# Optimization experiments

Hardware: AMD Instinct MI355X
Metric: run time of the kernel (lower is better)

## Reference

```python
import jax, jax.numpy as jnp
import numpy as np

EPS = 1e-7  # keras.backend.epsilon()


def setup_inputs() -> dict:
    key = jax.random.key(0)
    kx, kw, ku = jax.random.split(key, 3)
    B, S, F = 16, 4096, 512
    x = jax.random.normal(kx, (B, S, F), dtype=jnp.float32)
    # glorot-uniform-scaled weights
    limW = np.sqrt(6.0 / (F + F)).astype(np.float32)
    W = jax.random.uniform(kw, (F, F), dtype=jnp.float32, minval=-limW, maxval=limW)
    b = jnp.zeros((F,), dtype=jnp.float32)
    limu = np.sqrt(6.0 / (F + 1)).astype(np.float32)
    u = jax.random.uniform(ku, (F,), dtype=jnp.float32, minval=-limu, maxval=limu)
    return {"x": x, "W": W, "b": b, "u": u}


def reference(x, W, b, u):
    # x: [B,S,F]  W: [F,F]  b: [F]  u: [F]
    h = jnp.tanh(jnp.einsum('bsf,fg->bsg', x, W) + b)   # [B,S,F]
    scores = jnp.einsum('bsf,f->bs', h, u)              # [B,S]
    e = jnp.exp(scores)
    # NOTE: faithful to the source, normalization is GLOBAL over all B*S scores
    a = e / (jnp.sum(e) + EPS)                          # [B,S]
    out = jnp.einsum('bsf,bs->bf', x, a)                # [B,F] weighted-sum pool over steps
    return out
```

## Files before the change

kernel.cpp:

```cpp
#include <hip/hip_runtime.h>
#include <stdint.h>

#define EPSV 1e-7f
#define FDIM 512
#define BK 64
#define MT 128

typedef __bf16 bf16_t;
typedef bf16_t bf16x8 __attribute__((ext_vector_type(8)));
typedef unsigned short ushort8 __attribute__((ext_vector_type(8)));
typedef float f32x4 __attribute__((ext_vector_type(4)));

#define AS1 __attribute__((address_space(1)))
#define AS3 __attribute__((address_space(3)))

__device__ __forceinline__ unsigned short f2bf(float f) {
  union { float f; unsigned int u; } c; c.f = f;
  unsigned int u = c.u;
  unsigned int r = u + 0x7fffu + ((u >> 16) & 1u);
  return (unsigned short)(r >> 16);
}

__device__ __forceinline__ float fast_tanh(float x) {
  x = fminf(15.0f, fmaxf(-15.0f, x));
  float t = __expf(2.0f * x);
  return 1.0f - 2.0f * __builtin_amdgcn_rcpf(t + 1.0f);
}

__global__ void convert_W(const float* __restrict__ W, unsigned short* __restrict__ Wt) {
  int idx = blockIdx.x * 256 + threadIdx.x;
  int n = idx >> 9, k = idx & 511;
  Wt[idx] = f2bf(W[k * FDIM + n]);
}

__global__ __launch_bounds__(256, 2) void gemm_fused(
    const float* __restrict__ x, const unsigned short* __restrict__ Wt,
    const float* __restrict__ bvec, const float* __restrict__ uvec,
    float* __restrict__ out, float* __restrict__ sumE) {
  __shared__ unsigned short sA[MT * BK];
  __shared__ unsigned short sB[MT * BK];
  __shared__ float u_s[FDIM], b_s[FDIM];
  __shared__ float score_s[MT];
  __shared__ float e_s[MT];

  const int t = threadIdx.x;
  const int lane = t & 63;
  const int w = t >> 6;
  const int wm = w & 1;
  const int wn = w >> 1;
  const int quad = lane >> 4;
  const int l15 = lane & 15;
  const int m0 = blockIdx.x * MT;

  u_s[t] = uvec[t]; u_s[t + 256] = uvec[t + 256];
  b_s[t] = bvec[t]; b_s[t + 256] = bvec[t + 256];
  if (t < MT) score_s[t] = 0.0f;

  float sc[4][4];
#pragma unroll
  for (int mi = 0; mi < 4; ++mi)
#pragma unroll
    for (int r = 0; r < 4; ++r) sc[mi][r] = 0.0f;

  for (int nch = 0; nch < 4; ++nch) {
    f32x4 acc[4][4];
#pragma unroll
    for (int mi = 0; mi < 4; ++mi)
#pragma unroll
      for (int ni = 0; ni < 4; ++ni) acc[mi][ni] = (f32x4){0.f, 0.f, 0.f, 0.f};

    for (int kc = 0; kc < FDIM / BK; ++kc) {
      const int kbase = kc * BK;
#pragma unroll
      for (int p = 0; p < 4; ++p) {
        int slot = t + 256 * p;
        int row = slot >> 3;
        int j = (slot & 7) ^ (row & 7);
        const float* g = x + (size_t)(m0 + row) * FDIM + kbase + j * 8;
        float4 lo = *(const float4*)g;
        float4 hi = *(const float4*)(g + 4);
        ushort8 v;
        v[0] = f2bf(lo.x); v[1] = f2bf(lo.y); v[2] = f2bf(lo.z); v[3] = f2bf(lo.w);
        v[4] = f2bf(hi.x); v[5] = f2bf(hi.y); v[6] = f2bf(hi.z); v[7] = f2bf(hi.w);
        *(ushort8*)(void*)(sA + slot * 8) = v;
      }
#pragma unroll
      for (int i = 0; i < 4; ++i) {
        int nb = w * 32 + i * 8;
        int nl = nb + (lane >> 3);
        int j = (lane & 7) ^ (nl & 7);
        const unsigned short* g =
            Wt + (size_t)(nch * 128 + nl) * FDIM + kbase + j * 8;
        unsigned short* l = (unsigned short*)(sB + nb * 64);
        __builtin_amdgcn_global_load_lds((AS1 void*)(g), (AS3 void*)(l), 16, 0, 0);
      }
      __syncthreads();
#pragma unroll
      for (int ks = 0; ks < 2; ++ks) {
        bf16x8 af[4], bfr[4];
#pragma unroll
        for (int mi = 0; mi < 4; ++mi) {
          int row = wm * 64 + mi * 16 + l15;
          int phys = (ks * 4 + quad) ^ (row & 7);
          af[mi] = *(const bf16x8*)(const void*)(sA + row * 64 + phys * 8);
        }
#pragma unroll
        for (int ni = 0; ni < 4; ++ni) {
          int row = wn * 64 + ni * 16 + l15;
          int phys = (ks * 4 + quad) ^ (row & 7);
          bfr[ni] = *(const bf16x8*)(const void*)(sB + row * 64 + phys * 8);
        }
#pragma unroll
        for (int mi = 0; mi < 4; ++mi)
#pragma unroll
          for (int ni = 0; ni < 4; ++ni)
            acc[mi][ni] = __builtin_amdgcn_mfma_f32_16x16x32_bf16(
                af[mi], bfr[ni], acc[mi][ni], 0, 0, 0);
      }
      __syncthreads();
    }
#pragma unroll
    for (int ni = 0; ni < 4; ++ni) {
      int col = nch * 128 + wn * 64 + ni * 16 + l15;
      float uu = u_s[col], bb = b_s[col];
#pragma unroll
      for (int mi = 0; mi < 4; ++mi)
#pragma unroll
        for (int r = 0; r < 4; ++r)
          sc[mi][r] += uu * fast_tanh(acc[mi][ni][r] + bb);
    }
  }

#pragma unroll
  for (int mi = 0; mi < 4; ++mi)
#pragma unroll
    for (int r = 0; r < 4; ++r) {
      float v = sc[mi][r];
      v += __shfl_xor(v, 1); v += __shfl_xor(v, 2);
      v += __shfl_xor(v, 4); v += __shfl_xor(v, 8);
      if (l15 == 0)
        atomicAdd(&score_s[wm * 64 + mi * 16 + quad * 4 + r], v);
    }
  __syncthreads();

  if (t < MT) e_s[t] = __expf(score_s[t]);
  __syncthreads();

  if (t < 64) {
    float s = e_s[t] + e_s[t + 64];
    s += __shfl_xor(s, 1);  s += __shfl_xor(s, 2);  s += __shfl_xor(s, 4);
    s += __shfl_xor(s, 8);  s += __shfl_xor(s, 16); s += __shfl_xor(s, 32);
    if (t == 0) atomicAdd(sumE, s);
  }

  const int half = t >> 7;
  const int f4 = t & 127;
  float ax = 0.f, ay = 0.f, az = 0.f, aw = 0.f;
  for (int r = 0; r < 64; ++r) {
    int row = half * 64 + r;
    const float4 xv = *(const float4*)(x + (size_t)(m0 + row) * FDIM + f4 * 4);
    float wgt = e_s[row];
    ax += xv.x * wgt; ay += xv.y * wgt; az += xv.z * wgt; aw += xv.w * wgt;
  }
  const int bidx = m0 >> 12;
  float* op = out + bidx * FDIM + f4 * 4;
  atomicAdd(op + 0, ax); atomicAdd(op + 1, ay);
  atomicAdd(op + 2, az); atomicAdd(op + 3, aw);
}

__global__ void normalize_k(float* __restrict__ out, const float* __restrict__ sumE) {
  int i = blockIdx.x * 256 + threadIdx.x;
  out[i] *= 1.0f / (*sumE + EPSV);
}

extern "C" void kernel_launch(void* const* d_in, const int* in_sizes, int n_in,
                              void* d_out, int out_size, void* d_ws, size_t ws_size,
                              hipStream_t stream) {
  (void)in_sizes; (void)n_in; (void)ws_size;
  const float* x = (const float*)d_in[0];
  const float* W = (const float*)d_in[1];
  const float* b = (const float*)d_in[2];
  const float* u = (const float*)d_in[3];
  float* out = (float*)d_out;

  unsigned short* Wt = (unsigned short*)d_ws;
  float* sumE = (float*)((char*)d_ws + FDIM * FDIM * sizeof(unsigned short));

  hipMemsetAsync(d_out, 0, (size_t)out_size * sizeof(float), stream);
  hipMemsetAsync(sumE, 0, sizeof(float), stream);

  convert_W<<<dim3(FDIM * FDIM / 256), dim3(256), 0, stream>>>(W, Wt);
  gemm_fused<<<dim3(65536 / MT), dim3(256), 0, stream>>>(x, Wt, b, u, out, sumE);
  normalize_k<<<dim3(16 * FDIM / 256), dim3(256), 0, stream>>>(out, sumE);
}
```

Measured before the change: 283.4 us.

## Split fused GEMM into per-column-chunk blocks with separate exp and pool kernels

The fused kernel, where each block looped over all four 128-column chunks, is split so that each block handles one (row tile, column chunk) pair and writes partial scores. That gives 2048 blocks at higher occupancy. A new kernel sums the partials, exponentiates them and reduces the global sum. A separate pooling kernel then reads x again and folds in the normalization. W conversion now uses a shared-memory tiled transpose. The aim is more parallelism and better latency hiding. The cost is reading the fp32 x tile four times in the GEMM plus once more for pooling, plus extra launches and a score buffer round trip.

Measured after the change: 277.0 us. 2.3% less time.

```diff
diff --git a/kernel.cpp b/kernel.cpp
--- a/kernel.cpp
+++ b/kernel.cpp
@@ -4,7 +4,7 @@
 #define EPSV 1e-7f
 #define FDIM 512
 #define BK 64
-#define MT 128
+#define NROWS 65536
 
 typedef __bf16 bf16_t;
 typedef bf16_t bf16x8 __attribute__((ext_vector_type(8)));
@@ -28,20 +28,32 @@
 }
 
 __global__ void convert_W(const float* __restrict__ W, unsigned short* __restrict__ Wt) {
-  int idx = blockIdx.x * 256 + threadIdx.x;
-  int n = idx >> 9, k = idx & 511;
-  Wt[idx] = f2bf(W[k * FDIM + n]);
-}
-
-__global__ __launch_bounds__(256, 2) void gemm_fused(
+  __shared__ unsigned short tile[32][34];
+  const int t = threadIdx.x;
+  const int tx = t & 31, ty = t >> 5;
+  const int bn = blockIdx.x & 15, bk = blockIdx.x >> 4;
+  const int k0 = bk * 32, n0 = bn * 32;
+#pragma unroll
+  for (int i = 0; i < 4; ++i) {
+    int r = ty + i * 8;
+    tile[r][tx] = f2bf(W[(size_t)(k0 + r) * FDIM + n0 + tx]);
+  }
+  __syncthreads();
+#pragma unroll
+  for (int i = 0; i < 4; ++i) {
+    int r = ty + i * 8;
+    Wt[(size_t)(n0 + r) * FDIM + k0 + tx] = tile[tx][r];
+  }
+}
+
+__global__ __launch_bounds__(256, 4) void gemm_score(
     const float* __restrict__ x, const unsigned short* __restrict__ Wt,
     const float* __restrict__ bvec, const float* __restrict__ uvec,
-    float* __restrict__ out, float* __restrict__ sumE) {
-  __shared__ unsigned short sA[MT * BK];
-  __shared__ unsigned short sB[MT * BK];
-  __shared__ float u_s[FDIM], b_s[FDIM];
-  __shared__ float score_s[MT];
-  __shared__ float e_s[MT];
+    float* __restrict__ spart) {
+  __shared__ unsigned short sA[128 * BK];
+  __shared__ unsigned short sB[128 * BK];
+  __shared__ float score_s[128];
+  __shared__ float ub_s[128], bb_s[128];
 
   const int t = threadIdx.x;
   const int lane = t & 63;
@@ -50,87 +62,89 @@
   const int wn = w >> 1;
   const int quad = lane >> 4;
   const int l15 = lane & 15;
-  const int m0 = blockIdx.x * MT;
-
-  u_s[t] = uvec[t]; u_s[t + 256] = uvec[t + 256];
-  b_s[t] = bvec[t]; b_s[t + 256] = bvec[t + 256];
-  if (t < MT) score_s[t] = 0.0f;
+  const int rt = blockIdx.x >> 2;
+  const int nch = blockIdx.x & 3;
+  const int m0 = rt * 128;
+  const int col0 = nch * 128;
+
+  if (t < 128) {
+    score_s[t] = 0.0f;
+    ub_s[t] = uvec[col0 + t];
+    bb_s[t] = bvec[col0 + t];
+  }
+
+  f32x4 acc[4][4];
+#pragma unroll
+  for (int mi = 0; mi < 4; ++mi)
+#pragma unroll
+    for (int ni = 0; ni < 4; ++ni) acc[mi][ni] = (f32x4){0.f, 0.f, 0.f, 0.f};
+
+  for (int kc = 0; kc < FDIM / BK; ++kc) {
+    const int kbase = kc * BK;
+#pragma unroll
+    for (int p = 0; p < 4; ++p) {
+      int slot = t + 256 * p;
+      int row = slot >> 3;
+      int j = (slot & 7) ^ (row & 7);
+      const float* g = x + (size_t)(m0 + row) * FDIM + kbase + j * 8;
+      float4 lo = *(const float4*)g;
+      float4 hi = *(const float4*)(g + 4);
+      ushort8 v;
+      v[0] = f2bf(lo.x); v[1] = f2bf(lo.y); v[2] = f2bf(lo.z); v[3] = f2bf(lo.w);
+      v[4] = f2bf(hi.x); v[5] = f2bf(hi.y); v[6] = f2bf(hi.z); v[7] = f2bf(hi.w);
+      *(ushort8*)(void*)(sA + slot * 8) = v;
+    }
+#pragma unroll
+    for (int i = 0; i < 4; ++i) {
+      int nb = w * 32 + i * 8;
+      int nl = nb + (lane >> 3);
+      int j = (lane & 7) ^ (nl & 7);
+      const unsigned short* g =
+          Wt + (size_t)(col0 + nl) * FDIM + kbase + j * 8;
+      unsigned short* l = (unsigned short*)(sB + nb * 64);
+      __builtin_amdgcn_global_load_lds((AS1 void*)(g), (AS3 void*)(l), 16, 0, 0);
+    }
+    __syncthreads();
+#pragma unroll
+    for (int ks = 0; ks < 2; ++ks) {
+      bf16x8 af[4], bfr[4];
+#pragma unroll
+      for (int mi = 0; mi < 4; ++mi) {
+        int row = wm * 64 + mi * 16 + l15;
+        int phys = (ks * 4 + quad) ^ (row & 7);
+        af[mi] = *(const bf16x8*)(const void*)(sA + row * 64 + phys * 8);
+      }
+#pragma unroll
+      for (int ni = 0; ni < 4; ++ni) {
+        int row = wn * 64 + ni * 16 + l15;
+        int phys = (ks * 4 + quad) ^ (row & 7);
+        bfr[ni] = *(const bf16x8*)(const void*)(sB + row * 64 + phys * 8);
+      }
+#pragma unroll
+      for (int mi = 0; mi < 4; ++mi)
+#pragma unroll
+        for (int ni = 0; ni < 4; ++ni)
+          acc[mi][ni] = __builtin_amdgcn_mfma_f32_16x16x32_bf16(
+              af[mi], bfr[ni], acc[mi][ni], 0, 0, 0);
+    }
+    __syncthreads();
+  }
 
   float sc[4][4];
 #pragma unroll
   for (int mi = 0; mi < 4; ++mi)
 #pragma unroll
     for (int r = 0; r < 4; ++r) sc[mi][r] = 0.0f;
-
-  for (int nch = 0; nch < 4; ++nch) {
-    f32x4 acc[4][4];
+#pragma unroll
+  for (int ni = 0; ni < 4; ++ni) {
+    int cl = wn * 64 + ni * 16 + l15;
+    float uu = ub_s[cl], bb = bb_s[cl];
 #pragma unroll
     for (int mi = 0; mi < 4; ++mi)
 #pragma unroll
-      for (int ni = 0; ni < 4; ++ni) acc[mi][ni] = (f32x4){0.f, 0.f, 0.f, 0.f};
-
-    for (int kc = 0; kc < FDIM / BK; ++kc) {
-      const int kbase = kc * BK;
-#pragma unroll
-      for (int p = 0; p < 4; ++p) {
-        int slot = t + 256 * p;
-        int row = slot >> 3;
-        int j = (slot & 7) ^ (row & 7);
-        const float* g = x + (size_t)(m0 + row) * FDIM + kbase + j * 8;
-        float4 lo = *(const float4*)g;
-        float4 hi = *(const float4*)(g + 4);
-        ushort8 v;
-        v[0] = f2bf(lo.x); v[1] = f2bf(lo.y); v[2] = f2bf(lo.z); v[3] = f2bf(lo.w);
-        v[4] = f2bf(hi.x); v[5] = f2bf(hi.y); v[6] = f2bf(hi.z); v[7] = f2bf(hi.w);
-        *(ushort8*)(void*)(sA + slot * 8) = v;
-      }
-#pragma unroll
-      for (int i = 0; i < 4; ++i) {
-        int nb = w * 32 + i * 8;
-        int nl = nb + (lane >> 3);
-        int j = (lane & 7) ^ (nl & 7);
-        const unsigned short* g =
-            Wt + (size_t)(nch * 128 + nl) * FDIM + kbase + j * 8;
-        unsigned short* l = (unsigned short*)(sB + nb * 64);
-        __builtin_amdgcn_global_load_lds((AS1 void*)(g), (AS3 void*)(l), 16, 0, 0);
-      }
-      __syncthreads();
-#pragma unroll
-      for (int ks = 0; ks < 2; ++ks) {
-        bf16x8 af[4], bfr[4];
-#pragma unroll
-        for (int mi = 0; mi < 4; ++mi) {
-          int row = wm * 64 + mi * 16 + l15;
-          int phys = (ks * 4 + quad) ^ (row & 7);
-          af[mi] = *(const bf16x8*)(const void*)(sA + row * 64 + phys * 8);
-        }
-#pragma unroll
-        for (int ni = 0; ni < 4; ++ni) {
-          int row = wn * 64 + ni * 16 + l15;
-          int phys = (ks * 4 + quad) ^ (row & 7);
-          bfr[ni] = *(const bf16x8*)(const void*)(sB + row * 64 + phys * 8);
-        }
-#pragma unroll
-        for (int mi = 0; mi < 4; ++mi)
-#pragma unroll
-          for (int ni = 0; ni < 4; ++ni)
-            acc[mi][ni] = __builtin_amdgcn_mfma_f32_16x16x32_bf16(
-                af[mi], bfr[ni], acc[mi][ni], 0, 0, 0);
-      }
-      __syncthreads();
-    }
-#pragma unroll
-    for (int ni = 0; ni < 4; ++ni) {
-      int col = nch * 128 + wn * 64 + ni * 16 + l15;
-      float uu = u_s[col], bb = b_s[col];
-#pragma unroll
-      for (int mi = 0; mi < 4; ++mi)
-#pragma unroll
-        for (int r = 0; r < 4; ++r)
-          sc[mi][r] += uu * fast_tanh(acc[mi][ni][r] + bb);
-    }
-  }
-
+      for (int r = 0; r < 4; ++r)
+        sc[mi][r] += uu * fast_tanh(acc[mi][ni][r] + bb);
+  }
 #pragma unroll
   for (int mi = 0; mi < 4; ++mi)
 #pragma unroll
@@ -142,35 +156,53 @@
         atomicAdd(&score_s[wm * 64 + mi * 16 + quad * 4 + r], v);
     }
   __syncthreads();
-
-  if (t < MT) e_s[t] = __expf(score_s[t]);
-  __syncthreads();
-
-  if (t < 64) {
-    float s = e_s[t] + e_s[t + 64];
-    s += __shfl_xor(s, 1);  s += __shfl_xor(s, 2);  s += __shfl_xor(s, 4);
-    s += __shfl_xor(s, 8);  s += __shfl_xor(s, 16); s += __shfl_xor(s, 32);
-    if (t == 0) atomicAdd(sumE, s);
-  }
-
-  const int half = t >> 7;
-  const int f4 = t & 127;
+  if (t < 128) spart[(size_t)nch * NROWS + m0 + t] = score_s[t];
+}
+
+__global__ void score_exp(float* __restrict__ spart, float* __restrict__ sumE) {
+  __shared__ float ws_[4];
+  const int t = threadIdx.x;
+  const int i = blockIdx.x * 256 + t;
+  float s = spart[i] + spart[i + NROWS] + spart[i + 2 * NROWS] + spart[i + 3 * NROWS];
+  float e = __expf(s);
+  spart[i] = e;
+  float v = e;
+  v += __shfl_xor(v, 1);  v += __shfl_xor(v, 2);  v += __shfl_xor(v, 4);
+  v += __shfl_xor(v, 8);  v += __shfl_xor(v, 16); v += __shfl_xor(v, 32);
+  if ((t & 63) == 0) ws_[t >> 6] = v;
+  __syncthreads();
+  if (t == 0) atomicAdd(sumE, ws_[0] + ws_[1] + ws_[2] + ws_[3]);
+}
+
+__global__ __launch_bounds__(256) void pool_k(
+    const float* __restrict__ x, const float* __restrict__ e,
+    const float* __restrict__ sumE, float* __restrict__ out) {
+  __shared__ float e_s[128];
+  __shared__ float4 red[128];
+  const int t = threadIdx.x;
+  const int b = blockIdx.x >> 5, chunk = blockIdx.x & 31;
+  const int g0 = b * 4096 + chunk * 128;
+  if (t < 128) e_s[t] = e[g0 + t];
+  __syncthreads();
+  const int parity = t >> 7, f4 = t & 127;
   float ax = 0.f, ay = 0.f, az = 0.f, aw = 0.f;
   for (int r = 0; r < 64; ++r) {
-    int row = half * 64 + r;
-    const float4 xv = *(const float4*)(x + (size_t)(m0 + row) * FDIM + f4 * 4);
+    int row = r * 2 + parity;
+    const float4 xv = *(const float4*)(x + (size_t)(g0 + row) * FDIM + f4 * 4);
     float wgt = e_s[row];
     ax += xv.x * wgt; ay += xv.y * wgt; az += xv.z * wgt; aw += xv.w * wgt;
   }
-  const int bidx = m0 >> 12;
-  float* op = out + bidx * FDIM + f4 * 4;
-  atomicAdd(op + 0, ax); atomicAdd(op + 1, ay);
-  atomicAdd(op + 2, az); atomicAdd(op + 3, aw);
-}
-
-__global__ void normalize_k(float* __restrict__ out, const float* __restrict__ sumE) {
-  int i = blockIdx.x * 256 + threadIdx.x;
-  out[i] *= 1.0f / (*sumE + EPSV);
+  if (parity) red[f4] = (float4){ax, ay, az, aw};
+  __syncthreads();
+  if (!parity) {
+    float4 o = red[f4];
+    float inv = 1.0f / (*sumE + EPSV);
+    float* op = out + (size_t)b * FDIM + f4 * 4;
+    atomicAdd(op + 0, (ax + o.x) * inv);
+    atomicAdd(op + 1, (ay + o.y) * inv);
+    atomicAdd(op + 2, (az + o.z) * inv);
+    atomicAdd(op + 3, (aw + o.w) * inv);
+  }
 }
 
 extern "C" void kernel_launch(void* const* d_in, const int* in_sizes, int n_in,
@@ -184,12 +216,14 @@
   float* out = (float*)d_out;
 
   unsigned short* Wt = (unsigned short*)d_ws;
-  float* sumE = (float*)((char*)d_ws + FDIM * FDIM * sizeof(unsigned short));
+  float* spart = (float*)((char*)d_ws + (size_t)FDIM * FDIM * sizeof(unsigned short));
+  float* sumE = spart + 4 * NROWS;
 
   hipMemsetAsync(d_out, 0, (size_t)out_size * sizeof(float), stream);
   hipMemsetAsync(sumE, 0, sizeof(float), stream);
 
-  convert_W<<<dim3(FDIM * FDIM / 256), dim3(256), 0, stream>>>(W, Wt);
-  gemm_fused<<<dim3(65536 / MT), dim3(256), 0, stream>>>(x, Wt, b, u, out, sumE);
-  normalize_k<<<dim3(16 * FDIM / 256), dim3(256), 0, stream>>>(out, sumE);
-}
+  convert_W<<<dim3(256), dim3(256), 0, stream>>>(W, Wt);
+  gemm_score<<<dim3(2048), dim3(256), 0, stream>>>(x, Wt, b, u, spart);
+  score_exp<<<dim3(NROWS / 256), dim3(256), 0, stream>>>(spart, sumE);
+  pool_k<<<dim3(512), dim3(256), 0, stream>>>(x, spart, sumE, out);
+}
```
